# Performance work log

Hardware: AMD Instinct MI355X
Metric: run time of the kernel (lower is better)

The kernel has to match this reference:

```python
import jax, jax.numpy as jnp
import numpy as np

B, VS, VO = 16, 10475, 8192
K, PS, PO = 64, 1024, 2048


def setup_inputs() -> dict:
    key = jax.random.key(0)
    k1, k2, k3, k4, k5 = jax.random.split(key, 5)
    smplx_v = jax.random.normal(k1, (B, VS, 3), dtype=jnp.float32)
    object_v = jax.random.normal(k2, (B, VO, 3), dtype=jnp.float32)
    smpl_part_idx = jax.random.randint(k3, (K, PS), 0, VS, dtype=jnp.int64) if jax.config.jax_enable_x64 else jax.random.randint(k3, (K, PS), 0, VS, dtype=jnp.int32)
    obj_part_idx = jax.random.randint(k4, (K, PO), 0, VO, dtype=jnp.int32)
    batch_idx = jax.random.randint(k5, (K,), 0, B, dtype=jnp.int32)
    return {
        'smplx_v': smplx_v,
        'object_v': object_v,
        'smpl_part_idx': smpl_part_idx,
        'obj_part_idx': obj_part_idx,
        'batch_idx': batch_idx,
    }


def reference(smplx_v, object_v, smpl_part_idx, obj_part_idx, batch_idx):
    # Batched gather of per-pair contact vertex subsets.
    sc = smplx_v[batch_idx[:, None], smpl_part_idx]   # [K, PS, 3]
    oc = object_v[batch_idx[:, None], obj_part_idx]   # [K, PO, 3]
    # Pairwise Euclidean distances [K, PS, PO] (torch.norm of differences).
    diff = sc[:, :, None, :] - oc[:, None, :, :]
    d = jnp.sqrt(jnp.sum(diff * diff, axis=-1))
    # One-directional chamfer: min over object verts, mean over smpl verts,
    # then mean over all contact pairs (torch.stack(...).mean()).
    loss = jnp.mean(jnp.mean(jnp.min(d, axis=-1), axis=-1))
    return loss
```

## Files before the change

### kernel.cpp

```cpp
#include <hip/hip_runtime.h>
#include <float.h>
#include <math.h>

constexpr int B  = 16;
constexpr int VS = 10475;
constexpr int VO = 8192;
constexpr int K  = 64;
constexpr int PS = 1024;
constexpr int PO = 2048;

constexpr int BLK   = 1024;
constexpr int QPB   = 256;
constexpr int GRID  = K * (PS / QPB);
constexpr int NW    = 16;
constexpr int OHALF = PO / 2;
constexpr int NT    = OHALF / 32;

typedef float  v3f    __attribute__((ext_vector_type(3)));
typedef float  f32x16 __attribute__((ext_vector_type(16)));
typedef _Float16 half8 __attribute__((ext_vector_type(8)));
typedef unsigned int u32;
typedef u32 v4u __attribute__((ext_vector_type(4)));

__device__ __forceinline__ u32 pkh(_Float16 lo, _Float16 hi) {
    const unsigned short l = __builtin_bit_cast(unsigned short, lo);
    const unsigned short h = __builtin_bit_cast(unsigned short, hi);
    return ((u32)h << 16) | (u32)l;
}


__global__ __launch_bounds__(BLK)
void cl_onepass(const float* __restrict__ smplx_v,
                const float* __restrict__ object_v,
                const int*   __restrict__ spi,
                const int*   __restrict__ opi,
                const int*   __restrict__ bidx,
                float*       __restrict__ partial)
{
    __shared__ u32   so[(PO + 16) * 4];
    __shared__ float red[NW][32];
    __shared__ float s2lds[QPB];
    __shared__ float wsum[4];

    const int bk   = blockIdx.x;
    const int tid  = threadIdx.x;
    const int k    = bk >> 2;
    const int ic   = bk & 3;
    const int b    = bidx[k];
    const int wave = tid >> 6;
    const int lane = tid & 63;
    const int qg   = wave & 7;
    const int oh   = wave >> 3;

    const float* __restrict__ ov = object_v + (size_t)b * VO * 3;
    #pragma unroll
    for (int r = 0; r < PO / BLK; ++r) {
        const int j  = r * BLK + tid;
        const int oj = opi[k * PO + j];
        const v3f p  = *(const v3f*)(ov + 3 * (size_t)oj);
        const _Float16 hx = (_Float16)p.x, hy = (_Float16)p.y, hz = (_Float16)p.z;
        const float fx = (float)hx, fy = (float)hy, fz = (float)hz;
        const float w2 = 0.5f * (fx * fx + fy * fy + fz * fz);
        const _Float16 w2h = (_Float16)w2;
        const _Float16 w2l = (_Float16)(w2 - (float)w2h);
        const u32 d0 = pkh(hx, hy);
        *(v4u*)&so[j * 4] = (v4u){d0, pkh(hz, w2h), d0, pkh(hz, w2l)};
    }
    if (tid < 64) so[PO * 4 + tid] = 0;

    half8 afrag = (half8)(_Float16)0;
    if (lane < 32) {
        const int i  = ic * QPB + qg * 32 + lane;
        const int si = spi[k * PS + i];
        const v3f s  = *(const v3f*)(smplx_v + 3 * ((size_t)b * VS + si));
        const float s2 = s.x * s.x + s.y * s.y + s.z * s.z;
        const _Float16 shx = (_Float16)s.x, shy = (_Float16)s.y, shz = (_Float16)s.z;
        const _Float16 slx = (_Float16)(s.x - (float)shx);
        const _Float16 sly = (_Float16)(s.y - (float)shy);
        const _Float16 slz = (_Float16)(s.z - (float)shz);
        const _Float16 n1  = (_Float16)(-1.0f);
        afrag = (half8){shx, shy, shz, n1, slx, sly, slz, n1};
        if (wave < 8) s2lds[qg * 32 + lane] = s2;
    }
    __syncthreads();

    const u32* bp  = (lane < 32) ? &so[((size_t)oh * OHALF + (lane & 31)) * 4]
                                 : &so[PO * 4];
    const int  inc = (lane < 32) ? 32 * 4 : 0;

    f32x16 mint;
    #pragma unroll
    for (int i = 0; i < 16; ++i) mint[i] = FLT_MAX;

    #pragma unroll 4
    for (int t = 0; t < NT; ++t) {
        const half8 bfrag = *(const half8*)bp;
        f32x16 zc;
        #pragma unroll
        for (int i = 0; i < 16; ++i) zc[i] = 0.0f;
        const f32x16 d = __builtin_amdgcn_mfma_f32_32x32x16_f16(
            afrag, bfrag, zc, 0, 0, 0);
        #pragma unroll
        for (int i = 0; i < 16; ++i) mint[i] = fminf(mint[i], -d[i]);
        bp += inc;
    }

    #pragma unroll
    for (int m = 1; m <= 16; m <<= 1) {
        #pragma unroll
        for (int i = 0; i < 16; ++i)
            mint[i] = fminf(mint[i], __shfl_xor(mint[i], m, 64));
    }

    if ((lane & 31) == 0) {
        const int h = lane >> 5;
        #pragma unroll
        for (int reg = 0; reg < 16; ++reg) {
            const int row = (reg & 3) + 8 * (reg >> 2) + 4 * h;
            red[wave][row] = mint[reg];
        }
    }
    __syncthreads();

    float d = 0.0f;
    if (tid < QPB) {
        const int q2 = tid >> 5, row = tid & 31;
        const float m = fminf(red[q2][row], red[q2 + 8][row]);
        d = sqrtf(fmaxf(fmaf(2.0f, m, s2lds[tid]), 0.0f));
    }
    #pragma unroll
    for (int off = 32; off > 0; off >>= 1)
        d += __shfl_down(d, off, 64);
    if (lane == 0 && wave < 4) wsum[wave] = d;
    __syncthreads();
    if (tid == 0) partial[bk] = (wsum[0] + wsum[1]) + (wsum[2] + wsum[3]);
}


__global__ __launch_bounds__(64)
void cl_final(const float* __restrict__ partial, float* __restrict__ out)
{
    const int t = threadIdx.x;
    const float4 a = ((const float4*)partial)[t];
    float v = (a.x + a.y) + (a.z + a.w);
    #pragma unroll
    for (int off = 32; off > 0; off >>= 1)
        v += __shfl_down(v, off, 64);
    if (t == 0) out[0] = v * (1.0f / (float)(K * PS));
}


extern "C" void kernel_launch(void* const* d_in, const int* in_sizes, int n_in,
                              void* d_out, int out_size, void* d_ws, size_t ws_size,
                              hipStream_t stream)
{
    const float* smplx_v       = (const float*)d_in[0];
    const float* object_v      = (const float*)d_in[1];
    const int*   smpl_part_idx = (const int*)d_in[2];
    const int*   obj_part_idx  = (const int*)d_in[3];
    const int*   batch_idx     = (const int*)d_in[4];
    float*       out           = (float*)d_out;

    float* partial = (float*)d_ws;

    cl_onepass<<<GRID, BLK, 0, stream>>>(
        smplx_v, object_v, smpl_part_idx, obj_part_idx, batch_idx, partial);
    cl_final<<<1, 64, 0, stream>>>(partial, out);
}
```

Baseline: 16.59 us.

## Have each wave scan all object points and reduce mins in registers

Shrinks the block to 8 waves, each computing the min over the full object set for its 32 query points. This removes the LDS staging of partial mins, the s2 buffer and the cross-wave min combine. The row min is extracted from MFMA accumulator registers with lane shuffles. In exchange each wave runs a serial loop twice as long, and fewer threads share the object load, which reduces parallelism per block.

```diff
diff --git a/kernel.cpp b/kernel.cpp
--- a/kernel.cpp
+++ b/kernel.cpp
@@ -9,12 +9,11 @@
 constexpr int PS = 1024;
 constexpr int PO = 2048;
 
-constexpr int BLK   = 1024;
-constexpr int QPB   = 256;
-constexpr int GRID  = K * (PS / QPB);
-constexpr int NW    = 16;
-constexpr int OHALF = PO / 2;
-constexpr int NT    = OHALF / 32;
+constexpr int BLK  = 512;
+constexpr int QPB  = 256;
+constexpr int GRID = K * (PS / QPB);
+constexpr int NW   = 8;
+constexpr int NT   = PO / 32;
 
 typedef float  v3f    __attribute__((ext_vector_type(3)));
 typedef float  f32x16 __attribute__((ext_vector_type(16)));
@@ -38,9 +37,7 @@
                 float*       __restrict__ partial)
 {
     __shared__ u32   so[(PO + 16) * 4];
-    __shared__ float red[NW][32];
-    __shared__ float s2lds[QPB];
-    __shared__ float wsum[4];
+    __shared__ float wsum[NW];
 
     const int bk   = blockIdx.x;
     const int tid  = threadIdx.x;
@@ -49,8 +46,6 @@
     const int b    = bidx[k];
     const int wave = tid >> 6;
     const int lane = tid & 63;
-    const int qg   = wave & 7;
-    const int oh   = wave >> 3;
 
     const float* __restrict__ ov = object_v + (size_t)b * VO * 3;
     #pragma unroll
@@ -69,23 +64,22 @@
     if (tid < 64) so[PO * 4 + tid] = 0;
 
     half8 afrag = (half8)(_Float16)0;
+    float s2 = 0.0f;
     if (lane < 32) {
-        const int i  = ic * QPB + qg * 32 + lane;
+        const int i  = ic * QPB + wave * 32 + lane;
         const int si = spi[k * PS + i];
         const v3f s  = *(const v3f*)(smplx_v + 3 * ((size_t)b * VS + si));
-        const float s2 = s.x * s.x + s.y * s.y + s.z * s.z;
+        s2 = s.x * s.x + s.y * s.y + s.z * s.z;
         const _Float16 shx = (_Float16)s.x, shy = (_Float16)s.y, shz = (_Float16)s.z;
         const _Float16 slx = (_Float16)(s.x - (float)shx);
         const _Float16 sly = (_Float16)(s.y - (float)shy);
         const _Float16 slz = (_Float16)(s.z - (float)shz);
         const _Float16 n1  = (_Float16)(-1.0f);
         afrag = (half8){shx, shy, shz, n1, slx, sly, slz, n1};
-        if (wave < 8) s2lds[qg * 32 + lane] = s2;
     }
     __syncthreads();
 
-    const u32* bp  = (lane < 32) ? &so[((size_t)oh * OHALF + (lane & 31)) * 4]
-                                 : &so[PO * 4];
+    const u32* bp  = (lane < 32) ? &so[(lane & 31) * 4] : &so[PO * 4];
     const int  inc = (lane < 32) ? 32 * 4 : 0;
 
     f32x16 mint;
@@ -112,28 +106,32 @@
             mint[i] = fminf(mint[i], __shfl_xor(mint[i], m, 64));
     }
 
-    if ((lane & 31) == 0) {
-        const int h = lane >> 5;
-        #pragma unroll
-        for (int reg = 0; reg < 16; ++reg) {
-            const int row = (reg & 3) + 8 * (reg >> 2) + 4 * h;
-            red[wave][row] = mint[reg];
-        }
-    }
+    const int mm  = lane & 31;
+    const int reg = (mm & 3) | ((mm >> 3) << 2);
+    float sel = mint[0];
+    #pragma unroll
+    for (int r = 1; r < 16; ++r) sel = (reg == r) ? mint[r] : sel;
+    const float vA = __shfl(sel, mm, 64);
+    const float vB = __shfl(sel, mm + 32, 64);
+    const float d2m = ((mm >> 2) & 1) ? vB : vA;
+
+    float d = 0.0f;
+    if (lane < 32)
+        d = sqrtf(fmaxf(fmaf(2.0f, d2m, s2), 0.0f));
+
+    #pragma unroll
+    for (int m = 1; m <= 16; m <<= 1)
+        d += __shfl_xor(d, m, 64);
+    if (lane == 0) wsum[wave] = d;
     __syncthreads();
 
-    float d = 0.0f;
-    if (tid < QPB) {
-        const int q2 = tid >> 5, row = tid & 31;
-        const float m = fminf(red[q2][row], red[q2 + 8][row]);
-        d = sqrtf(fmaxf(fmaf(2.0f, m, s2lds[tid]), 0.0f));
+    if (tid < 64) {
+        float v = (tid < NW) ? wsum[tid] : 0.0f;
+        #pragma unroll
+        for (int off = 4; off > 0; off >>= 1)
+            v += __shfl_down(v, off, 64);
+        if (tid == 0) partial[bk] = v;
     }
-    #pragma unroll
-    for (int off = 32; off > 0; off >>= 1)
-        d += __shfl_down(d, off, 64);
-    if (lane == 0 && wave < 4) wsum[wave] = d;
-    __syncthreads();
-    if (tid == 0) partial[bk] = (wsum[0] + wsum[1]) + (wsum[2] + wsum[3]);
 }
 
 
```

Result: faster. 15.68 us (-5.5%).
